# Performance work log

Hardware: AMD Instinct MI355X
Metric: run time of the kernel (lower is better)

The kernel has to match this reference:

```python
import jax, jax.numpy as jnp
import numpy as np

S, B, D = 2048, 2, 1024
H = 16
DH = D // H
FF = 4096
EPS = 1e-5


def _layernorm(x, g, b):
    mu = jnp.mean(x, axis=-1, keepdims=True)
    var = jnp.var(x, axis=-1, keepdims=True)
    return (x - mu) * jax.lax.rsqrt(var + EPS) * g + b


def setup_inputs() -> dict:
    key = jax.random.key(0)
    ks = jax.random.split(key, 8)
    scale = 1.0 / np.sqrt(D)
    return {
        "x": jax.random.normal(ks[0], (S, B, D), dtype=jnp.float32),
        "wq": jax.random.normal(ks[1], (D, D), dtype=jnp.float32) * scale,
        "wk": jax.random.normal(ks[2], (D, D), dtype=jnp.float32) * scale,
        "wv": jax.random.normal(ks[3], (D, D), dtype=jnp.float32) * scale,
        "wo": jax.random.normal(ks[4], (D, D), dtype=jnp.float32) * scale,
        "ln1_g": jnp.ones((D,), jnp.float32),
        "ln1_b": jnp.zeros((D,), jnp.float32),
        "ln2_g": jnp.ones((D,), jnp.float32),
        "ln2_b": jnp.zeros((D,), jnp.float32),
        "w1": jax.random.normal(ks[5], (D, FF), dtype=jnp.float32) * scale,
        "b1": jnp.zeros((FF,), jnp.float32),
        "w2": jax.random.normal(ks[6], (FF, D), dtype=jnp.float32) * (1.0 / np.sqrt(FF)),
        "b2": jnp.zeros((D,), jnp.float32),
    }


def reference(x, wq, wk, wv, wo, ln1_g, ln1_b, ln2_g, ln2_b, w1, b1, w2, b2):
    # --- sublayer 0: pre-LN multi-head self-attention with residual ---
    # original loops per timestep with mask=False, i.e. full (non-causal)
    # attention over the whole sequence; vectorized here.
    y = _layernorm(x, ln1_g, ln1_b)                      # [S,B,D]
    q = (y @ wq).reshape(S, B, H, DH)
    k = (y @ wk).reshape(S, B, H, DH)
    v = (y @ wv).reshape(S, B, H, DH)
    scores = jnp.einsum("sbhd,tbhd->bhst", q, k) / np.sqrt(DH)  # [B,H,S,S]
    attn = jax.nn.softmax(scores, axis=-1)
    ctx = jnp.einsum("bhst,tbhd->sbhd", attn, v).reshape(S, B, D)
    x = x + ctx @ wo

    # --- sublayer 1: pre-LN position-wise FFN with residual ---
    z = _layernorm(x, ln2_g, ln2_b)
    h = jax.nn.relu(z @ w1 + b1)
    return x + h @ w2 + b2
```

## Files before the change

### kernel.cpp

```cpp
#include <hip/hip_runtime.h>
#include <hip/hip_bf16.h>
#include <stdint.h>


#define S_LEN 2048
#define BATCH 2
#define DMODEL 1024
#define NHEAD 16
#define DHEAD 64
#define FFDIM 4096
#define MROWS (S_LEN * BATCH)

typedef unsigned short u16;
typedef __attribute__((ext_vector_type(8))) __bf16 bf16x8;
typedef __attribute__((ext_vector_type(4))) float f32x4;
typedef __attribute__((ext_vector_type(4))) u16 u16x4;

__device__ inline u16 f2bf(float f) {
  union { float f; unsigned u; } v; v.f = f;
  unsigned r = v.u + 0x7fffu + ((v.u >> 16) & 1u);
  return (u16)(r >> 16);
}

__device__ inline f32x4 mfma16(bf16x8 a, bf16x8 b, f32x4 c) {
  return __builtin_amdgcn_mfma_f32_16x16x32_bf16(a, b, c, 0, 0, 0);
}

__device__ inline void gload_lds16(const u16* g, u16* l) {
  __builtin_amdgcn_global_load_lds(
      (const __attribute__((address_space(1))) unsigned int*)g,
      (__attribute__((address_space(3))) unsigned int*)l, 16, 0, 0);
}

__device__ inline uint32_t cvt_pk_bf16(float lo, float hi) {
  uint32_t r;
  asm("v_cvt_pk_bf16_f32 %0, %1, %2" : "=v"(r) : "v"(lo), "v"(hi));
  return r;
}

__global__ __launch_bounds__(256) void ln_kernel(const float* __restrict__ x,
                                                 const float* __restrict__ gam,
                                                 const float* __restrict__ bet,
                                                 u16* __restrict__ out) {
  int row = blockIdx.x;
  int tid = threadIdx.x;
  const float4* xr = (const float4*)(x + (size_t)row * DMODEL);
  float4 v = xr[tid];
  float s = v.x + v.y + v.z + v.w;
  float ss = v.x * v.x + v.y * v.y + v.z * v.z + v.w * v.w;
#pragma unroll
  for (int m = 1; m < 64; m <<= 1) {
    s += __shfl_xor(s, m);
    ss += __shfl_xor(ss, m);
  }
  __shared__ float red[8];
  int w = tid >> 6, lane = tid & 63;
  if (lane == 0) { red[w] = s; red[4 + w] = ss; }
  __syncthreads();
  s = red[0] + red[1] + red[2] + red[3];
  ss = red[4] + red[5] + red[6] + red[7];
  float mu = s * (1.f / DMODEL);
  float var = ss * (1.f / DMODEL) - mu * mu;
  float rstd = rsqrtf(var + 1e-5f);
  float4 gv = ((const float4*)gam)[tid];
  float4 bv = ((const float4*)bet)[tid];
  u16x4 o;
  o.x = f2bf((v.x - mu) * rstd * gv.x + bv.x);
  o.y = f2bf((v.y - mu) * rstd * gv.y + bv.y);
  o.z = f2bf((v.z - mu) * rstd * gv.z + bv.z);
  o.w = f2bf((v.w - mu) * rstd * gv.w + bv.w);
  *(u16x4*)(out + (size_t)row * DMODEL + tid * 4) = o;
}

__global__ __launch_bounds__(256) void transpose_cast(const float* __restrict__ in,
                                                      u16* __restrict__ out, int R, int C) {
  __shared__ u16 tile[32][33];
  int c0 = blockIdx.x * 32, r0 = blockIdx.y * 32;
  int tx = threadIdx.x & 31, grp = threadIdx.x >> 5;
#pragma unroll
  for (int i = 0; i < 4; i++) {
    int r = grp * 4 + i;
    tile[r][tx] = f2bf(in[(size_t)(r0 + r) * C + c0 + tx]);
  }
  __syncthreads();
#pragma unroll
  for (int i = 0; i < 4; i++) {
    int rr = grp * 4 + i;
    out[(size_t)(c0 + rr) * R + r0 + tx] = tile[tx][rr];
  }
}

__global__ __launch_bounds__(256) void transpose_v(const u16* __restrict__ qkv,
                                                   u16* __restrict__ vt) {
  __shared__ u16 tile[32][33];
  int bh = blockIdx.z;
  int b = bh >> 4;
  int s0 = blockIdx.x * 32, d0 = blockIdx.y * 32;
  int h = bh & 15;
  int tx = threadIdx.x & 31, grp = threadIdx.x >> 5;
#pragma unroll
  for (int i = 0; i < 4; i++) {
    int sl = grp * 4 + i;
    tile[sl][tx] = qkv[(size_t)((s0 + sl) * BATCH + b) * 3072 + 2048 + h * DHEAD + d0 + tx];
  }
  __syncthreads();
#pragma unroll
  for (int i = 0; i < 4; i++) {
    int dl = grp * 4 + i;
    vt[((size_t)bh * DHEAD + d0 + dl) * S_LEN + s0 + tx] = tile[tx][dl];
  }
}

template <int MODE, int BN>
__global__ __launch_bounds__(256) void gemm_bt(const u16* __restrict__ A,
                                               const u16* __restrict__ Bt, void* __restrict__ Cout,
                                               const float* __restrict__ bias,
                                               const float* __restrict__ res, int M, int N, int K) {
  __shared__ __align__(16) u16 As[2][128 * 64];
  __shared__ __align__(16) u16 Bs[2][BN * 64];

  int nwg = gridDim.x * gridDim.y;
  int f = blockIdx.y * gridDim.x + blockIdx.x;
  int nf = ((nwg & 7) == 0) ? ((f & 7) * (nwg >> 3) + (f >> 3)) : f;
  int bx = nf % gridDim.x, by = nf / gridDim.x;

  int bm0 = by * 128, bn0 = bx * BN;
  int tid = threadIdx.x, w = tid >> 6, lane = tid & 63;
  int g = lane >> 4, l15 = lane & 15;
  int lr = lane >> 3, ch = lane & 7;
  int srcch = (ch ^ lr) * 8;
  int wm = (w >> 1) * 64, wn = (w & 1) * (BN / 2);
  const int NJ = BN / 32;

  f32x4 acc[4][NJ];
#pragma unroll
  for (int i = 0; i < 4; i++)
#pragma unroll
    for (int j = 0; j < NJ; j++) {
      f32x4 z = {0.f, 0.f, 0.f, 0.f};
      acc[i][j] = z;
    }

  auto stage = [&](int k0, int buf) {
#pragma unroll
    for (int rd = 0; rd < 4; rd++) {
      int rb = (rd * 4 + w) * 8;
      gload_lds16(A + (size_t)(bm0 + rb + lr) * K + k0 + srcch, &As[buf][rb * 64]);
    }
#pragma unroll
    for (int rd = 0; rd < BN / 32; rd++) {
      int rb = (rd * 4 + w) * 8;
      gload_lds16(Bt + (size_t)(bn0 + rb + lr) * K + k0 + srcch, &Bs[buf][rb * 64]);
    }
  };

  int nkt = K >> 6;
  stage(0, 0);
  __syncthreads();

  for (int kt = 0; kt < nkt; ++kt) {
    int cur = kt & 1;
    if (kt + 1 < nkt) stage((kt + 1) << 6, cur ^ 1);
#pragma unroll
    for (int kk = 0; kk < 2; kk++) {
      bf16x8 af[4], bfr[NJ];
#pragma unroll
      for (int i = 0; i < 4; i++) {
        int row = wm + i * 16 + l15;
        af[i] = *(const bf16x8*)&As[cur][row * 64 + (((kk * 4 + g) ^ (row & 7)) * 8)];
      }
#pragma unroll
      for (int j = 0; j < NJ; j++) {
        int row = wn + j * 16 + l15;
        bfr[j] = *(const bf16x8*)&Bs[cur][row * 64 + (((kk * 4 + g) ^ (row & 7)) * 8)];
      }
#pragma unroll
      for (int i = 0; i < 4; i++)
#pragma unroll
        for (int j = 0; j < NJ; j++) acc[i][j] = mfma16(af[i], bfr[j], acc[i][j]);
    }
    __syncthreads();
  }

#pragma unroll
  for (int i = 0; i < 4; i++)
#pragma unroll
    for (int j = 0; j < NJ; j++) {
      int col = bn0 + wn + j * 16 + l15;
      float bval = (MODE == 2 || MODE == 3) ? bias[col] : 0.f;
#pragma unroll
      for (int r = 0; r < 4; r++) {
        int row = bm0 + wm + i * 16 + g * 4 + r;
        size_t idx = (size_t)row * N + col;
        float vacc = acc[i][j][r] + bval;
        if (MODE == 0)
          ((u16*)Cout)[idx] = f2bf(vacc);
        else if (MODE == 1)
          ((float*)Cout)[idx] = vacc + res[idx];
        else if (MODE == 2)
          ((u16*)Cout)[idx] = f2bf(fmaxf(vacc, 0.f));
        else
          ((float*)Cout)[idx] = vacc + res[idx];
      }
    }
}

__global__ __launch_bounds__(256) void attn_kernel(const u16* __restrict__ qkv,
                                                   const u16* __restrict__ vt,
                                                   u16* __restrict__ ctx) {
  int bh = blockIdx.y;
  int b = bh >> 4, h = bh & 15;
  int tid = threadIdx.x, w = tid >> 6, lane = tid & 63;
  int g = lane >> 4, l15 = lane & 15;
  int lr = lane >> 3, ch = lane & 7;
  int q0 = blockIdx.x * 128 + w * 32;
  const float SCALE = 0.125f * 1.44269504f;

  __shared__ __align__(16) u16 ks[2][64 * 64];
  __shared__ __align__(16) u16 vs[2][64 * 64];

  bf16x8 qf[2][2];
#pragma unroll
  for (int qs = 0; qs < 2; qs++) {
    const u16* qp = qkv + ((size_t)(q0 + qs * 16 + l15) * BATCH + b) * 3072 + h * DHEAD;
    qf[qs][0] = *(const bf16x8*)(qp + g * 8);
    qf[qs][1] = *(const bf16x8*)(qp + 32 + g * 8);
  }

  f32x4 accT[2][4];
#pragma unroll
  for (int qs = 0; qs < 2; qs++)
#pragma unroll
    for (int n = 0; n < 4; n++) {
      f32x4 z = {0.f, 0.f, 0.f, 0.f};
      accT[qs][n] = z;
    }
  float mrun[2] = {-1e30f, -1e30f}, lrun[2] = {0.f, 0.f};

  auto stage = [&](int t0, int buf) {
#pragma unroll
    for (int rd = 0; rd < 2; rd++) {
      int rb = w * 16 + rd * 8;
      int row = rb + lr;
      const u16* ksrc =
          qkv + ((size_t)(t0 + row) * BATCH + b) * 3072 + 1024 + h * DHEAD + (ch ^ lr) * 8;
      gload_lds16(ksrc, &ks[buf][rb * 64]);
      const u16* vsrc = vt + ((size_t)bh * DHEAD + row) * S_LEN + t0 + (ch ^ lr) * 8;
      gload_lds16(vsrc, &vs[buf][rb * 64]);
    }
  };

  stage(0, 0);
  __syncthreads();

  for (int it = 0; it < S_LEN / 64; ++it) {
    int cur = it & 1;
    if (it + 1 < S_LEN / 64) stage((it + 1) * 64, cur ^ 1);

    f32x4 scT[2][4];
#pragma unroll
    for (int tt = 0; tt < 4; tt++) {
      int row = tt * 16 + l15;
      bf16x8 kf0 = *(const bf16x8*)&ks[cur][row * 64 + ((g ^ (row & 7)) * 8)];
      bf16x8 kf1 = *(const bf16x8*)&ks[cur][row * 64 + (((4 + g) ^ (row & 7)) * 8)];
#pragma unroll
      for (int qs = 0; qs < 2; qs++) {
        f32x4 z = {0.f, 0.f, 0.f, 0.f};
        z = mfma16(kf0, qf[qs][0], z);
        z = mfma16(kf1, qf[qs][1], z);
        scT[qs][tt] = z * SCALE;
      }
    }

    bf16x8 pb[2][2];
#pragma unroll
    for (int qs = 0; qs < 2; qs++) {
      float pm = fmaxf(fmaxf(scT[qs][0][0], scT[qs][0][1]), fmaxf(scT[qs][0][2], scT[qs][0][3]));
#pragma unroll
      for (int tt = 1; tt < 4; tt++)
        pm = fmaxf(pm, fmaxf(fmaxf(scT[qs][tt][0], scT[qs][tt][1]),
                             fmaxf(scT[qs][tt][2], scT[qs][tt][3])));
      pm = fmaxf(pm, __shfl_xor(pm, 16));
      pm = fmaxf(pm, __shfl_xor(pm, 32));
      float mn = fmaxf(mrun[qs], pm);
      float al = __builtin_amdgcn_exp2f(mrun[qs] - mn);
      mrun[qs] = mn;
      float p[4][4];
      float psum = 0.f;
#pragma unroll
      for (int tt = 0; tt < 4; tt++)
#pragma unroll
        for (int r = 0; r < 4; r++) {
          p[tt][r] = __builtin_amdgcn_exp2f(scT[qs][tt][r] - mn);
          psum += p[tt][r];
        }
      psum += __shfl_xor(psum, 16);
      psum += __shfl_xor(psum, 32);
      lrun[qs] = lrun[qs] * al + psum;
#pragma unroll
      for (int n = 0; n < 4; n++) accT[qs][n] *= al;
      uint32_t P32[4][2];
#pragma unroll
      for (int tt = 0; tt < 4; tt++)
#pragma unroll
        for (int m = 0; m < 2; m++) P32[tt][m] = cvt_pk_bf16(p[tt][2 * m], p[tt][2 * m + 1]);
#pragma unroll
      for (int t5 = 0; t5 < 2; t5++)
#pragma unroll
        for (int m = 0; m < 2; m++) {
          asm("v_permlane32_swap_b32 %0, %1" : "+v"(P32[2 * t5][m]), "+v"(P32[2 * t5 + 1][m]));
          asm("v_permlane16_swap_b32 %0, %1" : "+v"(P32[2 * t5][m]), "+v"(P32[2 * t5 + 1][m]));
        }
#pragma unroll
      for (int s2 = 0; s2 < 2; s2++) {
        union { uint32_t u[4]; bf16x8 v; } uu;
        uu.u[0] = P32[2 * s2][0];
        uu.u[1] = P32[2 * s2][1];
        uu.u[2] = P32[2 * s2 + 1][0];
        uu.u[3] = P32[2 * s2 + 1][1];
        pb[qs][s2] = uu.v;
      }
    }

#pragma unroll
    for (int n = 0; n < 4; n++)
#pragma unroll
      for (int s2 = 0; s2 < 2; s2++) {
        int vrow = n * 16 + l15;
        int vchunk = (s2 * 4 + g) ^ (vrow & 7);
        bf16x8 vf = *(const bf16x8*)&vs[cur][vrow * 64 + vchunk * 8];
        accT[0][n] = mfma16(vf, pb[0][s2], accT[0][n]);
        accT[1][n] = mfma16(vf, pb[1][s2], accT[1][n]);
      }
    __syncthreads();
  }

#pragma unroll
  for (int qs = 0; qs < 2; qs++) {
    float inv = 1.f / lrun[qs];
    int srow = q0 + qs * 16 + l15;
#pragma unroll
    for (int n = 0; n < 4; n++) {
      u16x4 o;
      o.x = f2bf(accT[qs][n][0] * inv);
      o.y = f2bf(accT[qs][n][1] * inv);
      o.z = f2bf(accT[qs][n][2] * inv);
      o.w = f2bf(accT[qs][n][3] * inv);
      *(u16x4*)(ctx + ((size_t)srow * BATCH + b) * DMODEL + h * DHEAD + n * 16 + 4 * g) = o;
    }
  }
}

extern "C" void kernel_launch(void* const* d_in, const int* in_sizes, int n_in, void* d_out,
                              int out_size, void* d_ws, size_t ws_size, hipStream_t stream) {
  (void)in_sizes; (void)n_in; (void)out_size; (void)ws_size;
  const float* x    = (const float*)d_in[0];
  const float* wq   = (const float*)d_in[1];
  const float* wk   = (const float*)d_in[2];
  const float* wv   = (const float*)d_in[3];
  const float* wo   = (const float*)d_in[4];
  const float* ln1g = (const float*)d_in[5];
  const float* ln1b = (const float*)d_in[6];
  const float* ln2g = (const float*)d_in[7];
  const float* ln2b = (const float*)d_in[8];
  const float* w1   = (const float*)d_in[9];
  const float* b1   = (const float*)d_in[10];
  const float* w2   = (const float*)d_in[11];
  const float* b2   = (const float*)d_in[12];

  char* ws = (char*)d_ws;
  size_t off = 0;
  auto alloc = [&](size_t bytes) {
    void* p = ws + off;
    off += (bytes + 255) & ~(size_t)255;
    return p;
  };
  u16* yb    = (u16*)alloc((size_t)MROWS * DMODEL * 2);
  u16* wqkvt = (u16*)alloc((size_t)3072 * 1024 * 2);
  u16* wot   = (u16*)alloc((size_t)1024 * 1024 * 2);
  u16* w1t   = (u16*)alloc((size_t)4096 * 1024 * 2);
  u16* w2t   = (u16*)alloc((size_t)1024 * 4096 * 2);
  u16* qkvb  = (u16*)alloc((size_t)MROWS * 3072 * 2);
  u16* vtb   = (u16*)alloc((size_t)BATCH * NHEAD * DHEAD * S_LEN * 2);
  u16* ctxb  = (u16*)alloc((size_t)MROWS * DMODEL * 2);
  float* x1  = (float*)alloc((size_t)MROWS * DMODEL * 4);
  u16* zb    = (u16*)alloc((size_t)MROWS * DMODEL * 2);
  u16* hb    = (u16*)alloc((size_t)MROWS * FFDIM * 2);

  ln_kernel<<<MROWS, 256, 0, stream>>>(x, ln1g, ln1b, yb);
  transpose_cast<<<dim3(32, 32), 256, 0, stream>>>(wq, wqkvt, 1024, 1024);
  transpose_cast<<<dim3(32, 32), 256, 0, stream>>>(wk, wqkvt + 1024 * 1024, 1024, 1024);
  transpose_cast<<<dim3(32, 32), 256, 0, stream>>>(wv, wqkvt + 2 * 1024 * 1024, 1024, 1024);
  transpose_cast<<<dim3(32, 32), 256, 0, stream>>>(wo, wot, 1024, 1024);
  transpose_cast<<<dim3(128, 32), 256, 0, stream>>>(w1, w1t, 1024, 4096);
  transpose_cast<<<dim3(32, 128), 256, 0, stream>>>(w2, w2t, 4096, 1024);

  gemm_bt<0, 128><<<dim3(3072 / 128, 4096 / 128), 256, 0, stream>>>(yb, wqkvt, qkvb, nullptr,
                                                                    nullptr, 4096, 3072, 1024);
  transpose_v<<<dim3(64, 2, 32), 256, 0, stream>>>(qkvb, vtb);
  attn_kernel<<<dim3(16, 32), 256, 0, stream>>>(qkvb, vtb, ctxb);
  gemm_bt<1, 64><<<dim3(16, 32), 256, 0, stream>>>(ctxb, wot, x1, nullptr, x, 4096, 1024, 1024);

  ln_kernel<<<MROWS, 256, 0, stream>>>(x1, ln2g, ln2b, zb);
  gemm_bt<2, 128><<<dim3(32, 32), 256, 0, stream>>>(zb, w1t, hb, b1, nullptr, 4096, 4096, 1024);
  gemm_bt<3, 64><<<dim3(16, 32), 256, 0, stream>>>(hb, w2t, d_out, b2, x1, 4096, 1024, 4096);
}
```

Baseline: 267.4 us.

## Shrink attention work per wave, add lazy rescaling, and fine-grained waitcnt barriers

The attention kernel now gives each wave 16 query rows instead of 32 and launches twice as many workgroups, with the workgroup index remapped across the grid. It adds lazy softmax rescaling, so the running max and accumulators are only updated when a new max exceeds the old one by a threshold, and folds the scale into an fma. MFMA sections are wrapped in s_setprio. Both the GEMM and attention loops replace __syncthreads with explicit vmcnt waits plus raw s_barrier so the next tile's loads can stay in flight. The aim is more occupancy and less per-tile softmax and barrier overhead, at the cost of loading K/V tiles twice as often per query and relying on hand-counted vmcnt values being correct.

```diff
diff --git a/kernel.cpp b/kernel.cpp
--- a/kernel.cpp
+++ b/kernel.cpp
@@ -118,6 +118,7 @@
                                                const float* __restrict__ res, int M, int N, int K) {
   __shared__ __align__(16) u16 As[2][128 * 64];
   __shared__ __align__(16) u16 Bs[2][BN * 64];
+  constexpr int NLOADS = 4 + BN / 32;
 
   int nwg = gridDim.x * gridDim.y;
   int f = blockIdx.y * gridDim.x + blockIdx.x;
@@ -156,11 +157,18 @@
 
   int nkt = K >> 6;
   stage(0, 0);
-  __syncthreads();
+  asm volatile("s_waitcnt vmcnt(0)" ::: "memory");
+  __builtin_amdgcn_s_barrier();
 
   for (int kt = 0; kt < nkt; ++kt) {
     int cur = kt & 1;
-    if (kt + 1 < nkt) stage((kt + 1) << 6, cur ^ 1);
+    if (kt + 1 < nkt) {
+      stage((kt + 1) << 6, cur ^ 1);
+      asm volatile("s_waitcnt vmcnt(%0)" ::"n"(NLOADS) : "memory");
+    } else {
+      asm volatile("s_waitcnt vmcnt(0)" ::: "memory");
+    }
+    __builtin_amdgcn_s_barrier();
 #pragma unroll
     for (int kk = 0; kk < 2; kk++) {
       bf16x8 af[4], bfr[NJ];
@@ -179,7 +187,7 @@
 #pragma unroll
         for (int j = 0; j < NJ; j++) acc[i][j] = mfma16(af[i], bfr[j], acc[i][j]);
     }
-    __syncthreads();
+    __builtin_amdgcn_s_barrier();
   }
 
 #pragma unroll
@@ -208,34 +216,35 @@
 __global__ __launch_bounds__(256) void attn_kernel(const u16* __restrict__ qkv,
                                                    const u16* __restrict__ vt,
                                                    u16* __restrict__ ctx) {
-  int bh = blockIdx.y;
+  int nwg = gridDim.x * gridDim.y;
+  int f = blockIdx.y * gridDim.x + blockIdx.x;
+  int nf = (f & 7) * (nwg >> 3) + (f >> 3);
+  int qblk = nf % gridDim.x, bh = nf / gridDim.x;
   int b = bh >> 4, h = bh & 15;
   int tid = threadIdx.x, w = tid >> 6, lane = tid & 63;
   int g = lane >> 4, l15 = lane & 15;
   int lr = lane >> 3, ch = lane & 7;
-  int q0 = blockIdx.x * 128 + w * 32;
+  int q0 = qblk * 64 + w * 16;
   const float SCALE = 0.125f * 1.44269504f;
+  const float RAW_THR = 44.0f;
 
   __shared__ __align__(16) u16 ks[2][64 * 64];
   __shared__ __align__(16) u16 vs[2][64 * 64];
 
-  bf16x8 qf[2][2];
-#pragma unroll
-  for (int qs = 0; qs < 2; qs++) {
-    const u16* qp = qkv + ((size_t)(q0 + qs * 16 + l15) * BATCH + b) * 3072 + h * DHEAD;
-    qf[qs][0] = *(const bf16x8*)(qp + g * 8);
-    qf[qs][1] = *(const bf16x8*)(qp + 32 + g * 8);
-  }
-
-  f32x4 accT[2][4];
-#pragma unroll
-  for (int qs = 0; qs < 2; qs++)
-#pragma unroll
-    for (int n = 0; n < 4; n++) {
-      f32x4 z = {0.f, 0.f, 0.f, 0.f};
-      accT[qs][n] = z;
-    }
-  float mrun[2] = {-1e30f, -1e30f}, lrun[2] = {0.f, 0.f};
+  bf16x8 qf0, qf1;
+  {
+    const u16* qp = qkv + ((size_t)(q0 + l15) * BATCH + b) * 3072 + h * DHEAD;
+    qf0 = *(const bf16x8*)(qp + g * 8);
+    qf1 = *(const bf16x8*)(qp + 32 + g * 8);
+  }
+
+  f32x4 accT[4];
+#pragma unroll
+  for (int n = 0; n < 4; n++) {
+    f32x4 z = {0.f, 0.f, 0.f, 0.f};
+    accT[n] = z;
+  }
+  float mrun = -1e30f, lrun = 0.f;
 
   auto stage = [&](int t0, int buf) {
 #pragma unroll
@@ -251,103 +260,107 @@
   };
 
   stage(0, 0);
-  __syncthreads();
+  asm volatile("s_waitcnt vmcnt(0)" ::: "memory");
+  __builtin_amdgcn_s_barrier();
 
   for (int it = 0; it < S_LEN / 64; ++it) {
     int cur = it & 1;
-    if (it + 1 < S_LEN / 64) stage((it + 1) * 64, cur ^ 1);
-
-    f32x4 scT[2][4];
+    if (it + 1 < S_LEN / 64) {
+      stage((it + 1) * 64, cur ^ 1);
+      asm volatile("s_waitcnt vmcnt(4)" ::: "memory");
+    } else {
+      asm volatile("s_waitcnt vmcnt(0)" ::: "memory");
+    }
+    __builtin_amdgcn_s_barrier();
+
+    f32x4 scT[4];
 #pragma unroll
     for (int tt = 0; tt < 4; tt++) {
       int row = tt * 16 + l15;
       bf16x8 kf0 = *(const bf16x8*)&ks[cur][row * 64 + ((g ^ (row & 7)) * 8)];
       bf16x8 kf1 = *(const bf16x8*)&ks[cur][row * 64 + (((4 + g) ^ (row & 7)) * 8)];
-#pragma unroll
-      for (int qs = 0; qs < 2; qs++) {
-        f32x4 z = {0.f, 0.f, 0.f, 0.f};
-        z = mfma16(kf0, qf[qs][0], z);
-        z = mfma16(kf1, qf[qs][1], z);
-        scT[qs][tt] = z * SCALE;
+      f32x4 z = {0.f, 0.f, 0.f, 0.f};
+      __builtin_amdgcn_s_setprio(1);
+      z = mfma16(kf0, qf0, z);
+      z = mfma16(kf1, qf1, z);
+      __builtin_amdgcn_s_setprio(0);
+      scT[tt] = z;
+    }
+
+    float pm = fmaxf(fmaxf(scT[0][0], scT[0][1]), fmaxf(scT[0][2], scT[0][3]));
+#pragma unroll
+    for (int tt = 1; tt < 4; tt++)
+      pm = fmaxf(pm, fmaxf(fmaxf(scT[tt][0], scT[tt][1]), fmaxf(scT[tt][2], scT[tt][3])));
+    pm = fmaxf(pm, __shfl_xor(pm, 16));
+    pm = fmaxf(pm, __shfl_xor(pm, 32));
+    if (__any(pm > mrun + RAW_THR)) {
+      float mn = fmaxf(mrun, pm);
+      float al = __builtin_amdgcn_exp2f((mrun - mn) * SCALE);
+      mrun = mn;
+      lrun *= al;
+#pragma unroll
+      for (int n = 0; n < 4; n++) accT[n] *= al;
+    }
+    float mns = mrun * SCALE;
+    float p[4][4];
+    float psum = 0.f;
+#pragma unroll
+    for (int tt = 0; tt < 4; tt++)
+#pragma unroll
+      for (int r = 0; r < 4; r++) {
+        p[tt][r] = __builtin_amdgcn_exp2f(fmaf(scT[tt][r], SCALE, -mns));
+        psum += p[tt][r];
       }
-    }
-
-    bf16x8 pb[2][2];
-#pragma unroll
-    for (int qs = 0; qs < 2; qs++) {
-      float pm = fmaxf(fmaxf(scT[qs][0][0], scT[qs][0][1]), fmaxf(scT[qs][0][2], scT[qs][0][3]));
-#pragma unroll
-      for (int tt = 1; tt < 4; tt++)
-        pm = fmaxf(pm, fmaxf(fmaxf(scT[qs][tt][0], scT[qs][tt][1]),
-                             fmaxf(scT[qs][tt][2], scT[qs][tt][3])));
-      pm = fmaxf(pm, __shfl_xor(pm, 16));
-      pm = fmaxf(pm, __shfl_xor(pm, 32));
-      float mn = fmaxf(mrun[qs], pm);
-      float al = __builtin_amdgcn_exp2f(mrun[qs] - mn);
-      mrun[qs] = mn;
-      float p[4][4];
-      float psum = 0.f;
-#pragma unroll
-      for (int tt = 0; tt < 4; tt++)
-#pragma unroll
-        for (int r = 0; r < 4; r++) {
-          p[tt][r] = __builtin_amdgcn_exp2f(scT[qs][tt][r] - mn);
-          psum += p[tt][r];
-        }
-      psum += __shfl_xor(psum, 16);
-      psum += __shfl_xor(psum, 32);
-      lrun[qs] = lrun[qs] * al + psum;
-#pragma unroll
-      for (int n = 0; n < 4; n++) accT[qs][n] *= al;
-      uint32_t P32[4][2];
-#pragma unroll
-      for (int tt = 0; tt < 4; tt++)
-#pragma unroll
-        for (int m = 0; m < 2; m++) P32[tt][m] = cvt_pk_bf16(p[tt][2 * m], p[tt][2 * m + 1]);
-#pragma unroll
-      for (int t5 = 0; t5 < 2; t5++)
-#pragma unroll
-        for (int m = 0; m < 2; m++) {
-          asm("v_permlane32_swap_b32 %0, %1" : "+v"(P32[2 * t5][m]), "+v"(P32[2 * t5 + 1][m]));
-          asm("v_permlane16_swap_b32 %0, %1" : "+v"(P32[2 * t5][m]), "+v"(P32[2 * t5 + 1][m]));
-        }
-#pragma unroll
-      for (int s2 = 0; s2 < 2; s2++) {
-        union { uint32_t u[4]; bf16x8 v; } uu;
-        uu.u[0] = P32[2 * s2][0];
-        uu.u[1] = P32[2 * s2][1];
-        uu.u[2] = P32[2 * s2 + 1][0];
-        uu.u[3] = P32[2 * s2 + 1][1];
-        pb[qs][s2] = uu.v;
+    psum += __shfl_xor(psum, 16);
+    psum += __shfl_xor(psum, 32);
+    lrun += psum;
+
+    uint32_t P32[4][2];
+#pragma unroll
+    for (int tt = 0; tt < 4; tt++)
+#pragma unroll
+      for (int m = 0; m < 2; m++) P32[tt][m] = cvt_pk_bf16(p[tt][2 * m], p[tt][2 * m + 1]);
+#pragma unroll
+    for (int t5 = 0; t5 < 2; t5++)
+#pragma unroll
+      for (int m = 0; m < 2; m++) {
+        asm("v_permlane32_swap_b32 %0, %1" : "+v"(P32[2 * t5][m]), "+v"(P32[2 * t5 + 1][m]));
+        asm("v_permlane16_swap_b32 %0, %1" : "+v"(P32[2 * t5][m]), "+v"(P32[2 * t5 + 1][m]));
       }
-    }
-
-#pragma unroll
-    for (int n = 0; n < 4; n++)
-#pragma unroll
-      for (int s2 = 0; s2 < 2; s2++) {
-        int vrow = n * 16 + l15;
-        int vchunk = (s2 * 4 + g) ^ (vrow & 7);
-        bf16x8 vf = *(const bf16x8*)&vs[cur][vrow * 64 + vchunk * 8];
-        accT[0][n] = mfma16(vf, pb[0][s2], accT[0][n]);
-        accT[1][n] = mfma16(vf, pb[1][s2], accT[1][n]);
-      }
-    __syncthreads();
-  }
-
-#pragma unroll
-  for (int qs = 0; qs < 2; qs++) {
-    float inv = 1.f / lrun[qs];
-    int srow = q0 + qs * 16 + l15;
+    bf16x8 pb[2];
+#pragma unroll
+    for (int s2 = 0; s2 < 2; s2++) {
+      union { uint32_t u[4]; bf16x8 v; } uu;
+      uu.u[0] = P32[2 * s2][0];
+      uu.u[1] = P32[2 * s2][1];
+      uu.u[2] = P32[2 * s2 + 1][0];
+      uu.u[3] = P32[2 * s2 + 1][1];
+      pb[s2] = uu.v;
+    }
+
 #pragma unroll
     for (int n = 0; n < 4; n++) {
-      u16x4 o;
-      o.x = f2bf(accT[qs][n][0] * inv);
-      o.y = f2bf(accT[qs][n][1] * inv);
-      o.z = f2bf(accT[qs][n][2] * inv);
-      o.w = f2bf(accT[qs][n][3] * inv);
-      *(u16x4*)(ctx + ((size_t)srow * BATCH + b) * DMODEL + h * DHEAD + n * 16 + 4 * g) = o;
-    }
+      int vrow = n * 16 + l15;
+      bf16x8 vf0 = *(const bf16x8*)&vs[cur][vrow * 64 + ((g ^ (vrow & 7)) * 8)];
+      bf16x8 vf1 = *(const bf16x8*)&vs[cur][vrow * 64 + (((4 + g) ^ (vrow & 7)) * 8)];
+      __builtin_amdgcn_s_setprio(1);
+      accT[n] = mfma16(vf0, pb[0], accT[n]);
+      accT[n] = mfma16(vf1, pb[1], accT[n]);
+      __builtin_amdgcn_s_setprio(0);
+    }
+    __builtin_amdgcn_s_barrier();
+  }
+
+  float inv = 1.f / lrun;
+  int srow = q0 + l15;
+#pragma unroll
+  for (int n = 0; n < 4; n++) {
+    u16x4 o;
+    o.x = f2bf(accT[n][0] * inv);
+    o.y = f2bf(accT[n][1] * inv);
+    o.z = f2bf(accT[n][2] * inv);
+    o.w = f2bf(accT[n][3] * inv);
+    *(u16x4*)(ctx + ((size_t)srow * BATCH + b) * DMODEL + h * DHEAD + n * 16 + 4 * g) = o;
   }
 }
 
@@ -398,7 +411,7 @@
   gemm_bt<0, 128><<<dim3(3072 / 128, 4096 / 128), 256, 0, stream>>>(yb, wqkvt, qkvb, nullptr,
                                                                     nullptr, 4096, 3072, 1024);
   transpose_v<<<dim3(64, 2, 32), 256, 0, stream>>>(qkvb, vtb);
-  attn_kernel<<<dim3(16, 32), 256, 0, stream>>>(qkvb, vtb, ctxb);
+  attn_kernel<<<dim3(32, 32), 256, 0, stream>>>(qkvb, vtb, ctxb);
   gemm_bt<1, 64><<<dim3(16, 32), 256, 0, stream>>>(ctxb, wot, x1, nullptr, x, 4096, 1024, 1024);
 
   ln_kernel<<<MROWS, 256, 0, stream>>>(x1, ln2g, ln2b, zb);
```

New measurement: 260.4 us. -2.6%, faster.
